# Optimization experiments

Measured on AMD Instinct MI355X. Metric: run time of the kernel, lower is better.

## Reference

```python
import jax, jax.numpy as jnp
import numpy as np

B, S, H, NH = 2, 2048, 2048, 16
HD = H // NH
SCALE = 1.0 / np.sqrt(HD).astype(np.float32)


def setup_inputs() -> dict:
    key = jax.random.key(0)
    ks = jax.random.split(key, 10)
    std = 1.0 / np.sqrt(H)
    return {
        "x": jax.random.normal(ks[0], (B, S, H), dtype=jnp.float32),
        "attention_mask": jnp.zeros((B, 1, 1, S), dtype=jnp.float32),
        "Wq": jax.random.normal(ks[1], (H, H), dtype=jnp.float32) * std,
        "bq": jnp.zeros((H,), dtype=jnp.float32),
        "Wk": jax.random.normal(ks[2], (H, H), dtype=jnp.float32) * std,
        "bk": jnp.zeros((H,), dtype=jnp.float32),
        "Wv": jax.random.normal(ks[3], (H, H), dtype=jnp.float32) * std,
        "bv": jnp.zeros((H,), dtype=jnp.float32),
        "Wo": jax.random.normal(ks[4], (H, H), dtype=jnp.float32) * std,
        "bo": jnp.zeros((H,), dtype=jnp.float32),
    }


def _heads(t):
    # [B,S,H] -> [B,NH,S,HD]
    return t.reshape(B, S, NH, HD).transpose(0, 2, 1, 3)


def reference(x, attention_mask, Wq, bq, Wk, bk, Wv, bv, Wo, bo):
    q = _heads(x @ Wq.T + bq)
    k = _heads(x @ Wk.T + bk)
    v = _heads(x @ Wv.T + bv)
    scores = jnp.einsum("bhqd,bhkd->bhqk", q, k) * SCALE + attention_mask
    probs = jax.nn.softmax(scores, axis=-1)
    ctx = jnp.einsum("bhqk,bhkd->bhqd", probs, v)
    ctx = ctx.transpose(0, 2, 1, 3).reshape(B, S, H)
    return ctx @ Wo.T + bo
```

## Files before the change

### kernel.cpp

```cpp
#include <hip/hip_runtime.h>
#include <cstdint>
#include <cstddef>

#define B_   2
#define S_   2048
#define H_   2048
#define NH_  16
#define HD_  128
#define MM_  (B_ * S_)
#define K_   H_
#define SCALE_F 0.08838834764831845f
#define LOG2E_F 1.4426950408889634f
#define QSCALE_F (SCALE_F * LOG2E_F)

typedef __bf16 bf16_t;
typedef __attribute__((ext_vector_type(8))) __bf16 bf16x8;
typedef __attribute__((ext_vector_type(4))) __bf16 bf16x4;
typedef __attribute__((ext_vector_type(4))) float  f32x4;
typedef __attribute__((ext_vector_type(4))) float  floatx4;

static __device__ __forceinline__ f32x4 mfma_16x16x32(bf16x8 a, bf16x8 b, f32x4 c) {
  return __builtin_amdgcn_mfma_f32_16x16x32_bf16(a, b, c, 0, 0, 0);
}

static __device__ __forceinline__ void gl2lds16(const bf16_t* g, bf16_t* l) {
  __builtin_amdgcn_global_load_lds(
      (const __attribute__((address_space(1))) void*)g,
      (__attribute__((address_space(3))) void*)l, 16, 0, 0);
}

static __device__ __forceinline__ float exp2_hw(float x) {
  float r;
  asm("v_exp_f32 %0, %1" : "=v"(r) : "v"(x));
  return r;
}

__global__ void cvt6_f32_bf16(const float* __restrict__ x,
                              const float* __restrict__ w0, const float* __restrict__ w1,
                              const float* __restrict__ w2, const float* __restrict__ w3,
                              bf16_t* xo, bf16_t* o0, bf16_t* o1, bf16_t* o2, bf16_t* o3,
                              int n8) {
  const int yy = blockIdx.y;
  const float* in;
  bf16_t* out;
  if (yy == 0)      { in = x;                      out = xo; }
  else if (yy == 1) { in = x + (size_t)H_ * H_;    out = xo + (size_t)H_ * H_; }
  else if (yy == 2) { in = w0; out = o0; }
  else if (yy == 3) { in = w1; out = o1; }
  else if (yy == 4) { in = w2; out = o2; }
  else              { in = w3; out = o3; }
  int i = blockIdx.x * blockDim.x + threadIdx.x;
  const int stride = gridDim.x * blockDim.x;
  for (; i < n8; i += stride) {
    const floatx4* p = (const floatx4*)(in + (size_t)i * 8);
    floatx4 a = p[0], b = p[1];
    bf16x8 o;
    o[0] = (bf16_t)a.x; o[1] = (bf16_t)a.y; o[2] = (bf16_t)a.z; o[3] = (bf16_t)a.w;
    o[4] = (bf16_t)b.x; o[5] = (bf16_t)b.y; o[6] = (bf16_t)b.z; o[7] = (bf16_t)b.w;
    *(bf16x8*)(out + (size_t)i * 8) = o;
  }
}

template <int MODE, int NCOLS>
__global__ __launch_bounds__(256) void gemm_bt(
    const bf16_t* __restrict__ A,
    const bf16_t* __restrict__ W0, const bf16_t* __restrict__ W1, const bf16_t* __restrict__ W2,
    const float* __restrict__ bias0, const float* __restrict__ bias1, const float* __restrict__ bias2,
    bf16_t* __restrict__ dq, bf16_t* __restrict__ dk, bf16_t* __restrict__ dv,
    float* __restrict__ outf)
{
  __shared__ __align__(16) bf16_t Ash[128 * 64];
  __shared__ __align__(16) bf16_t Bsh[128 * 64];

  const int t = threadIdx.x;
  const int lane = t & 63;
  const int wid  = t >> 6;
  const int wm = wid >> 1, wn = wid & 1;

  const int lin = blockIdx.x;
  const int xcd = lin & 7;
  const int loc = lin >> 3;
  const int sr  = loc >> 5;
  const int l   = loc & 31;
  const int r_  = xcd * (NCOLS / 8) + sr;
  const int tm  = (r_ & 3) * 8 + (l & 7);
  const int nc  = (r_ >> 2) * 4 + (l >> 3);
  const int bm  = tm * 128;

  int bn;
  int wsel = 0;
  const bf16_t* Bw;
  const float*  bias;
  bf16_t* dsth = nullptr;
  if constexpr (MODE == 0) {
    wsel = nc >> 4;
    bn   = (nc & 15) * 128;
    Bw   = (wsel == 0) ? W0 : ((wsel == 1) ? W1 : W2);
    bias = (wsel == 0) ? bias0 : ((wsel == 1) ? bias1 : bias2);
    dsth = (wsel == 0) ? dq : ((wsel == 1) ? dk : dv);
  } else {
    bn = nc * 128;
    Bw = W0; bias = bias0;
  }

  const bf16_t* gA = A  + (size_t)bm * K_;
  const bf16_t* gB = Bw + (size_t)bn * K_;

  f32x4 acc[4][4] = {};

  #pragma unroll 1
  for (int k0 = 0; k0 < K_; k0 += 64) {
    #pragma unroll
    for (int j = 0; j < 4; ++j) {
      const int c = j * 256 + t;
      const int R = c >> 3;
      const int g = (c & 7) ^ (R & 7);
      bf16_t* la = Ash + (j * 256 + wid * 64) * 8;
      bf16_t* lb = Bsh + (j * 256 + wid * 64) * 8;
      gl2lds16(gA + (size_t)R * K_ + k0 + g * 8, la);
      gl2lds16(gB + (size_t)R * K_ + k0 + g * 8, lb);
    }
    __syncthreads();

    bf16x8 af[4][2], bfr[4][2];
    #pragma unroll
    for (int i = 0; i < 4; ++i)
      #pragma unroll
      for (int kk = 0; kk < 2; ++kk) {
        const int Ra = wm * 64 + i * 16 + (lane & 15);
        const int ca = (kk * 4 + (lane >> 4)) ^ (Ra & 7);
        af[i][kk] = *(const bf16x8*)&Ash[Ra * 64 + ca * 8];
        const int Rb = wn * 64 + i * 16 + (lane & 15);
        const int cb = (kk * 4 + (lane >> 4)) ^ (Rb & 7);
        bfr[i][kk] = *(const bf16x8*)&Bsh[Rb * 64 + cb * 8];
      }
    __builtin_amdgcn_s_setprio(1);
    #pragma unroll
    for (int kk = 0; kk < 2; ++kk)
      #pragma unroll
      for (int i = 0; i < 4; ++i)
        #pragma unroll
        for (int j2 = 0; j2 < 4; ++j2)
          acc[i][j2] = mfma_16x16x32(af[i][kk], bfr[j2][kk], acc[i][j2]);
    __builtin_amdgcn_s_setprio(0);
    __syncthreads();
  }

  const int row0 = bm + wm * 64 + (lane >> 4) * 4;
  const int col0 = bn + wn * 64 + (lane & 15);
  #pragma unroll
  for (int j2 = 0; j2 < 4; ++j2) {
    const int col = col0 + j2 * 16;
    const float bv = bias[col];
    #pragma unroll
    for (int i = 0; i < 4; ++i) {
      #pragma unroll
      for (int r = 0; r < 4; ++r) {
        const int row = row0 + i * 16 + r;
        float v = acc[i][j2][r] + bv;
        if constexpr (MODE == 0) {
          const int ss = row & (S_ - 1);
          const int dd = col & (HD_ - 1);
          const size_t bh = (size_t)((row >> 11) * NH_ + (col >> 7));
          if (wsel == 0) v *= QSCALE_F;
          size_t idx;
          if (wsel == 2) {
            const size_t t1 = bh * 32 + (ss >> 6);
            const size_t t2 = t1 * 8 + (dd >> 4);
            const size_t t3 = t2 * 2 + ((ss >> 5) & 1);
            const size_t ln = (size_t)((dd & 15) | (((ss >> 3) & 3) << 4));
            idx = (t3 * 64 + ln) * 8 + (size_t)(ss & 7);
          } else {
            const size_t t1 = bh * 128 + (ss >> 4);
            const size_t t2 = t1 * 4 + (dd >> 5);
            const size_t ln = (size_t)((ss & 15) | (((dd >> 3) & 3) << 4));
            idx = (t2 * 64 + ln) * 8 + (size_t)(dd & 7);
          }
          dsth[idx] = (bf16_t)v;
        } else {
          outf[(size_t)row * H_ + col] = v;
        }
      }
    }
  }
}

#define KVB 64
#define NT_ (S_ / KVB)
#define TILE_E 8192

__global__ __launch_bounds__(128, 2) void attn_kernel(
    const bf16_t* __restrict__ Qf, const bf16_t* __restrict__ Kf,
    const bf16_t* __restrict__ Vf, const float* __restrict__ mask,
    bf16_t* __restrict__ ctx)
{
  __shared__ __align__(16) bf16_t Klds[TILE_E];
  __shared__ __align__(16) bf16_t Vlds[TILE_E];
  __shared__ __align__(16) bf16_t Plds[2][2048];

  const int t = threadIdx.x;
  const int lane = t & 63;
  const int wid  = t >> 6;
  const int g    = lane >> 4;

  const int orig = blockIdx.x;
  const int wg = (orig & 7) * 128 + (orig >> 3);
  const int qt = wg & 31;
  const int bh = wg >> 5;
  const int b  = bh >> 4;
  const int h  = bh & 15;
  const int q0 = qt * 64 + wid * 32;

  const bf16_t* Kh0 = Kf + (size_t)bh * (NT_ * TILE_E);
  const bf16_t* Vh0 = Vf + (size_t)bh * (NT_ * TILE_E);
  const float*  mg  = mask + (size_t)b * S_;

  const bf16_t* Qt = Qf + (((size_t)bh * 128 + (q0 >> 4)) * 4) * 512;
  bf16x8 qf[2][4];
  #pragma unroll
  for (int mh = 0; mh < 2; ++mh)
    #pragma unroll
    for (int ks = 0; ks < 4; ++ks)
      qf[mh][ks] = *(const bf16x8*)&Qt[((mh * 4 + ks) * 64 + lane) * 8];

  f32x4 acc[2][8] = {};
  float m_run[2] = {-INFINITY, -INFINITY};
  float l_run[2] = {0.0f, 0.0f};

  char* Pw = (char*)&Plds[wid][0];

  auto stage = [&](int it) {
    const bf16_t* Ksrc = Kh0 + (size_t)it * TILE_E;
    const bf16_t* Vsrc = Vh0 + (size_t)it * TILE_E;
    #pragma unroll
    for (int i = 0; i < 8; ++i) {
      const int base = (i * 128 + wid * 64) * 8;
      gl2lds16(Ksrc + base + lane * 8, &Klds[base]);
      gl2lds16(Vsrc + base + lane * 8, &Vlds[base]);
    }
  };

  #pragma unroll 1
  for (int it = 0; it < NT_; ++it) {
    stage(it);

    const int kv0 = it * KVB;
    floatx4 mv[4];
    #pragma unroll
    for (int ns = 0; ns < 4; ++ns)
      mv[ns] = *(const floatx4*)&mg[kv0 + ns * 16 + g * 4];

    __syncthreads();

    f32x4 sacc[2][4] = {};
    #pragma unroll
    for (int ns = 0; ns < 4; ++ns) {
      #pragma unroll
      for (int ks = 0; ks < 4; ++ks) {
        const bf16x8 kf = *(const bf16x8*)&Klds[((ns * 4 + ks) * 64 + lane) * 8];
        __builtin_amdgcn_s_setprio(1);
        sacc[0][ns] = mfma_16x16x32(kf, qf[0][ks], sacc[0][ns]);
        sacc[1][ns] = mfma_16x16x32(kf, qf[1][ks], sacc[1][ns]);
        __builtin_amdgcn_s_setprio(0);
      }
    }

    float tmax[2];
    #pragma unroll
    for (int mh = 0; mh < 2; ++mh) {
      float tm = -INFINITY;
      #pragma unroll
      for (int ns = 0; ns < 4; ++ns)
        #pragma unroll
        for (int r = 0; r < 4; ++r) {
          sacc[mh][ns][r] += mv[ns][r];
          tm = fmaxf(tm, sacc[mh][ns][r]);
        }
      tm = fmaxf(tm, __shfl_xor(tm, 16));
      tm = fmaxf(tm, __shfl_xor(tm, 32));
      tmax[mh] = tm;
    }

    const bool small = (tmax[0] <= m_run[0] + 8.0f) && (tmax[1] <= m_run[1] + 8.0f);
    if (!__all(small)) {
      #pragma unroll
      for (int mh = 0; mh < 2; ++mh) {
        const float mnew = fmaxf(m_run[mh], tmax[mh]);
        const float scl  = exp2_hw(m_run[mh] - mnew);
        m_run[mh] = mnew;
        l_run[mh] *= scl;
        #pragma unroll
        for (int ds = 0; ds < 8; ++ds)
          #pragma unroll
          for (int r = 0; r < 4; ++r)
            acc[mh][ds][r] *= scl;
      }
    }

    float rs[2] = {0.0f, 0.0f};
    #pragma unroll
    for (int mh = 0; mh < 2; ++mh) {
      #pragma unroll
      for (int ns = 0; ns < 4; ++ns) {
        bf16x4 pk;
        #pragma unroll
        for (int r = 0; r < 4; ++r) {
          const float p = exp2_hw(sacc[mh][ns][r] - m_run[mh]);
          rs[mh] += p;
          pk[r] = (bf16_t)p;
        }
        const int L = (lane & 15) | ((((ns & 1) << 1) | (g >> 1)) << 4);
        const int byte = mh * 2048 + ((ns >> 1) << 10) + L * 16 + (g & 1) * 8;
        *(bf16x4*)(Pw + byte) = pk;
      }
    }

    bf16x8 pf[2][2];
    #pragma unroll
    for (int mh = 0; mh < 2; ++mh)
      #pragma unroll
      for (int ks2 = 0; ks2 < 2; ++ks2)
        pf[mh][ks2] = *(const bf16x8*)(Pw + mh * 2048 + ks2 * 1024 + lane * 16);

    #pragma unroll
    for (int ds = 0; ds < 8; ++ds) {
      const bf16x8 vf0 = *(const bf16x8*)&Vlds[((ds * 2 + 0) * 64 + lane) * 8];
      const bf16x8 vf1 = *(const bf16x8*)&Vlds[((ds * 2 + 1) * 64 + lane) * 8];
      __builtin_amdgcn_s_setprio(1);
      #pragma unroll
      for (int mh = 0; mh < 2; ++mh) {
        acc[mh][ds] = mfma_16x16x32(vf0, pf[mh][0], acc[mh][ds]);
        acc[mh][ds] = mfma_16x16x32(vf1, pf[mh][1], acc[mh][ds]);
      }
      __builtin_amdgcn_s_setprio(0);
    }

    #pragma unroll
    for (int mh = 0; mh < 2; ++mh) {
      rs[mh] += __shfl_xor(rs[mh], 16);
      rs[mh] += __shfl_xor(rs[mh], 32);
      l_run[mh] += rs[mh];
    }

    __syncthreads();
  }

  #pragma unroll
  for (int mh = 0; mh < 2; ++mh) {
    const int q = q0 + mh * 16 + (lane & 15);
    const float inv = 1.0f / l_run[mh];
    #pragma unroll
    for (int ds = 0; ds < 8; ++ds) {
      bf16x4 o;
      #pragma unroll
      for (int r = 0; r < 4; ++r)
        o[r] = (bf16_t)(acc[mh][ds][r] * inv);
      *(bf16x4*)&ctx[((size_t)(b * S_ + q)) * H_ + h * HD_ + ds * 16 + g * 4] = o;
    }
  }
}

extern "C" void kernel_launch(void* const* d_in, const int* in_sizes, int n_in,
                              void* d_out, int out_size, void* d_ws, size_t ws_size,
                              hipStream_t stream) {
  (void)in_sizes; (void)n_in; (void)out_size; (void)ws_size;
  const float* x    = (const float*)d_in[0];
  const float* mask = (const float*)d_in[1];
  const float* Wq   = (const float*)d_in[2];
  const float* bq   = (const float*)d_in[3];
  const float* Wk   = (const float*)d_in[4];
  const float* bk   = (const float*)d_in[5];
  const float* Wv   = (const float*)d_in[6];
  const float* bv   = (const float*)d_in[7];
  const float* Wo   = (const float*)d_in[8];
  const float* bo   = (const float*)d_in[9];
  float* out = (float*)d_out;

  const size_t nX = (size_t)MM_ * H_;
  const size_t nW = (size_t)H_ * H_;

  bf16_t* xbf = (bf16_t*)d_ws;
  bf16_t* wqb = xbf + nX;
  bf16_t* wkb = wqb + nW;
  bf16_t* wvb = wkb + nW;
  bf16_t* wob = wvb + nW;
  bf16_t* qf  = wob + nW;
  bf16_t* kf  = qf + nX;
  bf16_t* vf  = kf + nX;
  bf16_t* cxb = vf + nX;

  cvt6_f32_bf16<<<dim3(512, 6), 256, 0, stream>>>(
      x, Wq, Wk, Wv, Wo, xbf, wqb, wkb, wvb, wob, (int)(nW / 8));

  gemm_bt<0, 48><<<32 * 48, 256, 0, stream>>>(
      xbf, wqb, wkb, wvb, bq, bk, bv, qf, kf, vf, nullptr);

  attn_kernel<<<1024, 128, 0, stream>>>(qf, kf, vf, mask, cxb);

  gemm_bt<1, 16><<<32 * 16, 256, 0, stream>>>(
      cxb, wob, nullptr, nullptr, bo, nullptr, nullptr, nullptr, nullptr, nullptr, out);
}
```

Before: 280.5 us.

## Double-buffer GEMM LDS tiles to overlap global loads with MFMA compute

Splits the shared-memory A/B tiles into two buffers and issues the next k-tile's global-to-LDS loads before computing on the current one. A partial vmcnt wait and raw s_barrier replace the full __syncthreads, so load latency can overlap the MFMA work. LDS use doubles to 64KB per block, which may lower occupancy. Correctness depends on the vmcnt count matching the 8 loads issued per stage.

```diff
diff --git a/kernel.cpp b/kernel.cpp
--- a/kernel.cpp
+++ b/kernel.cpp
@@ -34,6 +34,8 @@
   asm("v_exp_f32 %0, %1" : "=v"(r) : "v"(x));
   return r;
 }
+
+#define VMW(n) asm volatile("s_waitcnt vmcnt(" #n ")" ::: "memory")
 
 __global__ void cvt6_f32_bf16(const float* __restrict__ x,
                               const float* __restrict__ w0, const float* __restrict__ w1,
@@ -69,8 +71,8 @@
     bf16_t* __restrict__ dq, bf16_t* __restrict__ dk, bf16_t* __restrict__ dv,
     float* __restrict__ outf)
 {
-  __shared__ __align__(16) bf16_t Ash[128 * 64];
-  __shared__ __align__(16) bf16_t Bsh[128 * 64];
+  __shared__ __align__(16) bf16_t Ash[2][128 * 64];
+  __shared__ __align__(16) bf16_t Bsh[2][128 * 64];
 
   const int t = threadIdx.x;
   const int lane = t & 63;
@@ -106,21 +108,37 @@
   const bf16_t* gA = A  + (size_t)bm * K_;
   const bf16_t* gB = Bw + (size_t)bn * K_;
 
-  f32x4 acc[4][4] = {};
-
-  #pragma unroll 1
-  for (int k0 = 0; k0 < K_; k0 += 64) {
+  auto stage = [&](int kt, int b) {
+    const int k0 = kt * 64;
     #pragma unroll
     for (int j = 0; j < 4; ++j) {
       const int c = j * 256 + t;
       const int R = c >> 3;
       const int g = (c & 7) ^ (R & 7);
-      bf16_t* la = Ash + (j * 256 + wid * 64) * 8;
-      bf16_t* lb = Bsh + (j * 256 + wid * 64) * 8;
-      gl2lds16(gA + (size_t)R * K_ + k0 + g * 8, la);
-      gl2lds16(gB + (size_t)R * K_ + k0 + g * 8, lb);
-    }
-    __syncthreads();
+      gl2lds16(gA + (size_t)R * K_ + k0 + g * 8, &Ash[b][(j * 256 + wid * 64) * 8]);
+      gl2lds16(gB + (size_t)R * K_ + k0 + g * 8, &Bsh[b][(j * 256 + wid * 64) * 8]);
+    }
+  };
+
+  f32x4 acc[4][4] = {};
+
+  stage(0, 0);
+
+  constexpr int NTK = K_ / 64;
+  #pragma unroll 1
+  for (int kt = 0; kt < NTK; ++kt) {
+    const int cur = kt & 1;
+    if (kt + 1 < NTK) {
+      stage(kt + 1, cur ^ 1);
+      VMW(8);
+    } else {
+      VMW(0);
+    }
+    __builtin_amdgcn_s_barrier();
+    __builtin_amdgcn_sched_barrier(0);
+
+    const bf16_t* Al = &Ash[cur][0];
+    const bf16_t* Bl = &Bsh[cur][0];
 
     bf16x8 af[4][2], bfr[4][2];
     #pragma unroll
@@ -129,10 +147,10 @@
       for (int kk = 0; kk < 2; ++kk) {
         const int Ra = wm * 64 + i * 16 + (lane & 15);
         const int ca = (kk * 4 + (lane >> 4)) ^ (Ra & 7);
-        af[i][kk] = *(const bf16x8*)&Ash[Ra * 64 + ca * 8];
+        af[i][kk] = *(const bf16x8*)&Al[Ra * 64 + ca * 8];
         const int Rb = wn * 64 + i * 16 + (lane & 15);
         const int cb = (kk * 4 + (lane >> 4)) ^ (Rb & 7);
-        bfr[i][kk] = *(const bf16x8*)&Bsh[Rb * 64 + cb * 8];
+        bfr[i][kk] = *(const bf16x8*)&Bl[Rb * 64 + cb * 8];
       }
     __builtin_amdgcn_s_setprio(1);
     #pragma unroll
@@ -143,7 +161,8 @@
         for (int j2 = 0; j2 < 4; ++j2)
           acc[i][j2] = mfma_16x16x32(af[i][kk], bfr[j2][kk], acc[i][j2]);
     __builtin_amdgcn_s_setprio(0);
-    __syncthreads();
+    __builtin_amdgcn_sched_barrier(0);
+    __builtin_amdgcn_s_barrier();
   }
 
   const int row0 = bm + wm * 64 + (lane >> 4) * 4;
```

Result: no change. 282.8 us (+0.8%).

## Enlarge GEMM block tile to 256x128 and simplify XCD tile mapping

Applied to the files above, without the earlier changes.

Doubles the M dimension of each GEMM workgroup tile from 128 to 256 rows. Each wave now computes 128x64 outputs with 32 accumulators, loading B fragments once and reusing them across two A sub-tiles. The block-to-tile mapping is simplified so each XCD owns a fixed set of column tiles and walks the M tiles. The goal is more arithmetic per LDS/global load, at the cost of higher register and LDS use, lower occupancy, and half as many blocks (768 and 256), which may underfill the GPU for the output projection.

```diff
diff --git a/kernel.cpp b/kernel.cpp
--- a/kernel.cpp
+++ b/kernel.cpp
@@ -69,7 +69,7 @@
     bf16_t* __restrict__ dq, bf16_t* __restrict__ dk, bf16_t* __restrict__ dv,
     float* __restrict__ outf)
 {
-  __shared__ __align__(16) bf16_t Ash[128 * 64];
+  __shared__ __align__(16) bf16_t Ash[256 * 64];
   __shared__ __align__(16) bf16_t Bsh[128 * 64];
 
   const int t = threadIdx.x;
@@ -80,12 +80,10 @@
   const int lin = blockIdx.x;
   const int xcd = lin & 7;
   const int loc = lin >> 3;
-  const int sr  = loc >> 5;
-  const int l   = loc & 31;
-  const int r_  = xcd * (NCOLS / 8) + sr;
-  const int tm  = (r_ & 3) * 8 + (l & 7);
-  const int nc  = (r_ >> 2) * 4 + (l >> 3);
-  const int bm  = tm * 128;
+  constexpr int NCPX = NCOLS / 8;
+  const int nc  = xcd * NCPX + (loc % NCPX);
+  const int tm  = loc / NCPX;
+  const int bm  = tm * 256;
 
   int bn;
   int wsel = 0;
@@ -106,58 +104,72 @@
   const bf16_t* gA = A  + (size_t)bm * K_;
   const bf16_t* gB = Bw + (size_t)bn * K_;
 
-  f32x4 acc[4][4] = {};
+  f32x4 acc[8][4] = {};
 
   #pragma unroll 1
   for (int k0 = 0; k0 < K_; k0 += 64) {
+    #pragma unroll
+    for (int j = 0; j < 8; ++j) {
+      const int c = j * 256 + t;
+      const int R = c >> 3;
+      const int g = (c & 7) ^ (R & 7);
+      gl2lds16(gA + (size_t)R * K_ + k0 + g * 8, &Ash[(j * 256 + wid * 64) * 8]);
+    }
     #pragma unroll
     for (int j = 0; j < 4; ++j) {
       const int c = j * 256 + t;
       const int R = c >> 3;
       const int g = (c & 7) ^ (R & 7);
-      bf16_t* la = Ash + (j * 256 + wid * 64) * 8;
-      bf16_t* lb = Bsh + (j * 256 + wid * 64) * 8;
-      gl2lds16(gA + (size_t)R * K_ + k0 + g * 8, la);
-      gl2lds16(gB + (size_t)R * K_ + k0 + g * 8, lb);
+      gl2lds16(gB + (size_t)R * K_ + k0 + g * 8, &Bsh[(j * 256 + wid * 64) * 8]);
     }
     __syncthreads();
 
-    bf16x8 af[4][2], bfr[4][2];
-    #pragma unroll
-    for (int i = 0; i < 4; ++i)
+    bf16x8 bfr[4][2];
+    #pragma unroll
+    for (int n = 0; n < 4; ++n)
       #pragma unroll
       for (int kk = 0; kk < 2; ++kk) {
-        const int Ra = wm * 64 + i * 16 + (lane & 15);
-        const int ca = (kk * 4 + (lane >> 4)) ^ (Ra & 7);
-        af[i][kk] = *(const bf16x8*)&Ash[Ra * 64 + ca * 8];
-        const int Rb = wn * 64 + i * 16 + (lane & 15);
+        const int Rb = wn * 64 + n * 16 + (lane & 15);
         const int cb = (kk * 4 + (lane >> 4)) ^ (Rb & 7);
-        bfr[i][kk] = *(const bf16x8*)&Bsh[Rb * 64 + cb * 8];
-      }
-    __builtin_amdgcn_s_setprio(1);
-    #pragma unroll
-    for (int kk = 0; kk < 2; ++kk)
+        bfr[n][kk] = *(const bf16x8*)&Bsh[Rb * 64 + cb * 8];
+      }
+
+    #pragma unroll
+    for (int qm = 0; qm < 2; ++qm) {
+      bf16x8 af[4][2];
       #pragma unroll
       for (int i = 0; i < 4; ++i)
         #pragma unroll
-        for (int j2 = 0; j2 < 4; ++j2)
-          acc[i][j2] = mfma_16x16x32(af[i][kk], bfr[j2][kk], acc[i][j2]);
-    __builtin_amdgcn_s_setprio(0);
+        for (int kk = 0; kk < 2; ++kk) {
+          const int Ra = wm * 128 + qm * 64 + i * 16 + (lane & 15);
+          const int ca = (kk * 4 + (lane >> 4)) ^ (Ra & 7);
+          af[i][kk] = *(const bf16x8*)&Ash[Ra * 64 + ca * 8];
+        }
+      __builtin_amdgcn_s_setprio(1);
+      #pragma unroll
+      for (int kk = 0; kk < 2; ++kk)
+        #pragma unroll
+        for (int i = 0; i < 4; ++i)
+          #pragma unroll
+          for (int n = 0; n < 4; ++n)
+            acc[qm * 4 + i][n] = mfma_16x16x32(af[i][kk], bfr[n][kk], acc[qm * 4 + i][n]);
+      __builtin_amdgcn_s_setprio(0);
+    }
     __syncthreads();
   }
 
-  const int row0 = bm + wm * 64 + (lane >> 4) * 4;
   const int col0 = bn + wn * 64 + (lane & 15);
   #pragma unroll
   for (int j2 = 0; j2 < 4; ++j2) {
     const int col = col0 + j2 * 16;
     const float bv = bias[col];
     #pragma unroll
-    for (int i = 0; i < 4; ++i) {
+    for (int ai = 0; ai < 8; ++ai) {
+      const int rowbase = bm + wm * 128 + (ai >> 2) * 64 + (ai & 3) * 16 + (lane >> 4) * 4;
       #pragma unroll
       for (int r = 0; r < 4; ++r) {
-        const int row = row0 + i * 16 + r;
-        float v = acc[i][j2][r] + bv;
+        const int row = rowbase + r;
+        float v = acc[ai][j2][r] + bv;
         if constexpr (MODE == 0) {
           const int ss = row & (S_ - 1);
           const int dd = col & (HD_ - 1);
@@ -392,11 +404,11 @@
   cvt6_f32_bf16<<<dim3(512, 6), 256, 0, stream>>>(
       x, Wq, Wk, Wv, Wo, xbf, wqb, wkb, wvb, wob, (int)(nW / 8));
 
-  gemm_bt<0, 48><<<32 * 48, 256, 0, stream>>>(
+  gemm_bt<0, 48><<<768, 256, 0, stream>>>(
       xbf, wqb, wkb, wvb, bq, bk, bv, qf, kf, vf, nullptr);
 
   attn_kernel<<<1024, 128, 0, stream>>>(qf, kf, vf, mask, cxb);
 
-  gemm_bt<1, 16><<<32 * 16, 256, 0, stream>>>(
+  gemm_bt<1, 16><<<256, 256, 0, stream>>>(
       cxb, wob, nullptr, nullptr, bo, nullptr, nullptr, nullptr, nullptr, nullptr, out);
 }
```

Result: slower. 395.5 us (+41.0%).
